# Performance work log

Measured on AMD Instinct MI355X. Metric: run time of the kernel, lower is better.

## Reference

```python
import jax, jax.numpy as jnp
import numpy as np

N = 16384
IN_FEATS = 128
HIDDEN = 128
OUT_FEATS = 64


def setup_inputs() -> dict:
    key = jax.random.key(0)
    ks = jax.random.split(key, 8)
    x = jax.random.normal(ks[0], (N, IN_FEATS), dtype=jnp.float32)
    adj = jax.random.uniform(ks[1], (N, N), dtype=jnp.float32)
    def glorot(k, shape):
        lim = 1.0 / np.sqrt(shape[0])
        return jax.random.uniform(k, shape, minval=-lim, maxval=lim, dtype=jnp.float32)
    W1 = glorot(ks[2], (IN_FEATS, HIDDEN))
    b1 = jnp.zeros((HIDDEN,), dtype=jnp.float32)
    W2 = glorot(ks[3], (HIDDEN, OUT_FEATS))
    b2 = jnp.zeros((OUT_FEATS,), dtype=jnp.float32)
    W_out = glorot(ks[4], (OUT_FEATS, 1))
    b_out = jnp.zeros((1,), dtype=jnp.float32)
    return {"x": x, "adj": adj, "W1": W1, "b1": b1, "W2": W2, "b2": b2,
            "W_out": W_out, "b_out": b_out}


def _gcn_layer(x, adj, W, b):
    # support = x @ W ; out = adj @ support + b  (standard GraphConvLayer)
    return adj @ (x @ W) + b


def reference(x, adj, W1, b1, W2, b2, W_out, b_out):
    h = jax.nn.relu(_gcn_layer(x, adj, W1, b1))      # [N, hidden]
    h = _gcn_layer(h, adj, W2, b2)                   # [N, out_feats]
    pooled = h.sum(axis=0)                           # [out_feats] graph readout
    return pooled @ W_out + b_out                    # [1]
```

## Files before the change

### kernel.cpp

```cpp
#include <hip/hip_runtime.h>
#include <hip/hip_bf16.h>
#include <stdint.h>

#define NN   16384
#define FI   128
#define FH   128
#define FO   64

#define BM   32
#define BK   64
#define LDK  72
#define KHALF (NN / 2)
#define NTH  (KHALF / BK)
#define NPART 512

typedef float f32x4 __attribute__((ext_vector_type(4)));
typedef short s16x8 __attribute__((ext_vector_type(8)));
typedef short s16x4 __attribute__((ext_vector_type(4)));

__device__ __forceinline__ unsigned short f2bf(float f) {
    union { float f; unsigned u; } v; v.f = f;
    unsigned u = v.u;
    return (unsigned short)((u + 0x7FFFu + ((u >> 16) & 1u)) >> 16);
}

__global__ __launch_bounds__(256) void k1_s1t(const float* __restrict__ x,
                                              const float* __restrict__ W1,
                                              unsigned short* __restrict__ S1T) {
    __shared__ float w1s[FI][FH];
    __shared__ float xs[64][132];

    const int t  = threadIdx.x;
    const int b  = blockIdx.x;
    const int k0 = b * 64;

    float* wflat = &w1s[0][0];
    for (int i = t; i < FI * FH; i += 256) wflat[i] = W1[i];

    #pragma unroll
    for (int s = 0; s < 8; ++s) {
        int idx = t + 256 * s;
        int r   = idx >> 5;
        int f4  = idx & 31;
        f32x4 vv = *(const f32x4*)(x + (size_t)(k0 + r) * FI + f4 * 4);
        *(f32x4*)(&xs[r][f4 * 4]) = vv;
    }
    __syncthreads();

    const int w = t >> 6;
    const int l = t & 63;

    float acc[32];
    #pragma unroll
    for (int j = 0; j < 32; ++j) acc[j] = 0.f;

    for (int f4 = 0; f4 < 32; ++f4) {
        f32x4 xv = *(const f32x4*)(&xs[l][f4 * 4]);
        #pragma unroll
        for (int e = 0; e < 4; ++e) {
            const int f = f4 * 4 + e;
            #pragma unroll
            for (int cth = 0; cth < 8; ++cth) {
                f32x4 wv = *(const f32x4*)(&w1s[f][w * 32 + cth * 4]);
                acc[cth * 4 + 0] += xv[e] * wv[0];
                acc[cth * 4 + 1] += xv[e] * wv[1];
                acc[cth * 4 + 2] += xv[e] * wv[2];
                acc[cth * 4 + 3] += xv[e] * wv[3];
            }
        }
    }

    const int k = k0 + l;
    #pragma unroll
    for (int j = 0; j < 32; ++j) {
        const int n = w * 32 + j;
        S1T[(size_t)n * NN + k] = f2bf(acc[j]);
    }
}

__global__ __launch_bounds__(256, 4) void k2_agg(const float* __restrict__ adj,
                                                 const unsigned short* __restrict__ S1T,
                                                 float* __restrict__ Tpart,
                                                 float* __restrict__ cpart) {
    __shared__ unsigned short aA[2][BM][LDK];
    __shared__ unsigned short bBs[FH][LDK];
    __shared__ float cs[4][BK];

    const int  t    = threadIdx.x;
    const int  rb   = blockIdx.x >> 1;
    const int  kh   = blockIdx.x & 1;
    const long m0   = (long)rb * BM;
    const long k0   = (long)kh * KHALF;
    const int  w    = t >> 6;
    const int  l    = t & 63;
    const int  ar   = t >> 4;
    const int  ac4  = t & 15;
    const int  sn   = t >> 3;
    const int  sch  = t & 7;
    const int  m    = l & 15;
    const int  quad = l >> 4;

    f32x4 acc[2][2];
    #pragma unroll
    for (int i = 0; i < 2; ++i)
        #pragma unroll
        for (int j = 0; j < 2; ++j) acc[i][j] = (f32x4){0.f, 0.f, 0.f, 0.f};

    f32x4 paX0, paX1, paY0, paY1;
    s16x8 psX[4], psY[4];

#define BAR() do {                                                                \
    asm volatile("s_waitcnt lgkmcnt(0)" ::: "memory");                            \
    __builtin_amdgcn_s_barrier();                                                 \
} while (0)

#define LOAD(PA0, PA1, PS, J) do {                                                \
    const long koff_ = k0 + (long)(J) * BK;                                       \
    PA0 = *(const f32x4*)(adj + (m0 + ar) * NN + koff_ + ac4 * 4);                \
    PA1 = *(const f32x4*)(adj + (m0 + ar + 16) * NN + koff_ + ac4 * 4);           \
    _Pragma("unroll")                                                             \
    for (int s_ = 0; s_ < 4; ++s_)                                                \
        PS[s_] = *(const s16x8*)(S1T + (size_t)(sn + 32 * s_) * NN + koff_ + sch * 8); \
} while (0)

#define CSUM_STAGEA(SB, PA0, PA1) do {                                            \
    f32x4 pv_;                                                                    \
    _Pragma("unroll")                                                             \
    for (int j_ = 0; j_ < 4; ++j_) {                                              \
        float p_ = PA0[j_] + PA1[j_];                                             \
        p_ += __shfl_xor(p_, 16);                                                 \
        p_ += __shfl_xor(p_, 32);                                                 \
        pv_[j_] = p_;                                                             \
    }                                                                             \
    if (l < 16) *(f32x4*)(&cs[w][l * 4]) = pv_;                                   \
    s16x4 q0_, q1_;                                                               \
    _Pragma("unroll")                                                             \
    for (int j_ = 0; j_ < 4; ++j_) {                                              \
        q0_[j_] = (short)f2bf(PA0[j_]);                                           \
        q1_[j_] = (short)f2bf(PA1[j_]);                                           \
    }                                                                             \
    *(s16x4*)(&aA[SB][ar][ac4 * 4])      = q0_;                                   \
    *(s16x4*)(&aA[SB][ar + 16][ac4 * 4]) = q1_;                                   \
} while (0)

#define STAGEB(PS) do {                                                           \
    _Pragma("unroll")                                                             \
    for (int s_ = 0; s_ < 4; ++s_)                                                \
        *(s16x8*)(&bBs[sn + 32 * s_][sch * 8]) = PS[s_];                          \
} while (0)

#define FLUSH(J) do {                                                             \
    if (t < BK)                                                                   \
        cpart[(size_t)rb * NN + k0 + (long)(J) * BK + t] =                        \
            cs[0][t] + cs[1][t] + cs[2][t] + cs[3][t];                            \
} while (0)

#define COMPUTE(SB) do {                                                          \
    _Pragma("unroll")                                                             \
    for (int ks = 0; ks < 2; ++ks) {                                              \
        s16x8 af_[2], bf_[2];                                                     \
        _Pragma("unroll")                                                         \
        for (int mt = 0; mt < 2; ++mt)                                            \
            af_[mt] = *(const s16x8*)(&aA[SB][mt * 16 + m][ks * 32 + quad * 8]);  \
        _Pragma("unroll")                                                         \
        for (int nt = 0; nt < 2; ++nt)                                            \
            bf_[nt] = *(const s16x8*)(&bBs[w * 32 + nt * 16 + m][ks * 32 + quad * 8]); \
        _Pragma("unroll")                                                         \
        for (int mt = 0; mt < 2; ++mt)                                            \
            _Pragma("unroll")                                                     \
            for (int nt = 0; nt < 2; ++nt)                                        \
                acc[mt][nt] = __builtin_amdgcn_mfma_f32_16x16x32_bf16(            \
                    af_[mt], bf_[nt], acc[mt][nt], 0, 0, 0);                      \
    }                                                                             \
} while (0)

    LOAD(paX0, paX1, psX, 0);
    LOAD(paY0, paY1, psY, 1);
    CSUM_STAGEA(0, paX0, paX1);
    STAGEB(psX);
    BAR();
    FLUSH(0);
    BAR();

    for (int j = 0; j < NTH; j += 2) {
        if (j + 2 < NTH) LOAD(paX0, paX1, psX, j + 2);
        COMPUTE(0);
        CSUM_STAGEA(1, paY0, paY1);
        BAR();
        STAGEB(psY);
        FLUSH(j + 1);
        BAR();

        if (j + 3 < NTH) LOAD(paY0, paY1, psY, j + 3);
        COMPUTE(1);
        if (j + 2 < NTH) CSUM_STAGEA(0, paX0, paX1);
        BAR();
        if (j + 2 < NTH) {
            STAGEB(psX);
            FLUSH(j + 2);
        }
        BAR();
    }

#undef BAR
#undef LOAD
#undef CSUM_STAGEA
#undef STAGEB
#undef FLUSH
#undef COMPUTE

    float* Tp = Tpart + (size_t)kh * NN * FH;
    #pragma unroll
    for (int mt = 0; mt < 2; ++mt)
        #pragma unroll
        for (int nt = 0; nt < 2; ++nt) {
            const int col = w * 32 + nt * 16 + m;
            #pragma unroll
            for (int r = 0; r < 4; ++r) {
                const long row = m0 + mt * 16 + quad * 4 + r;
                Tp[row * FH + col] = acc[mt][nt][r];
            }
        }
}

__global__ __launch_bounds__(256) void k3_v(const float* __restrict__ Tpart,
                                            const float* __restrict__ cpart,
                                            const float* __restrict__ b1,
                                            float* __restrict__ v) {
    __shared__ float vp[FH];
    __shared__ float cw[4][64];
    __shared__ float cloc[64];

    const int t = threadIdx.x;
    const int b = blockIdx.x;
    const int w = t >> 6;
    const int l = t & 63;

    float s = 0.f;
    #pragma unroll 8
    for (int i = 0; i < NPART / 4; ++i)
        s += cpart[(size_t)(w + 4 * i) * NN + b * 64 + l];
    cw[w][l] = s;
    if (t < FH) vp[t] = 0.f;
    __syncthreads();
    if (t < 64) cloc[t] = cw[0][t] + cw[1][t] + cw[2][t] + cw[3][t];
    __syncthreads();

    const int kk = t >> 2;
    const int mq = t & 3;
    const int k  = b * 64 + kk;
    const float ck = cloc[kk];

    #pragma unroll
    for (int j4 = 0; j4 < 8; ++j4) {
        f32x4 t0 = *(const f32x4*)(Tpart + (size_t)k * FH + mq * 32 + j4 * 4);
        f32x4 t1 = *(const f32x4*)(Tpart + ((size_t)NN + k) * FH + mq * 32 + j4 * 4);
        f32x4 bv = *(const f32x4*)(b1 + mq * 32 + j4 * 4);
        #pragma unroll
        for (int e = 0; e < 4; ++e) {
            float h = t0[e] + t1[e] + bv[e];
            h = h > 0.f ? h : 0.f;
            atomicAdd(&vp[mq * 32 + j4 * 4 + e], ck * h);
        }
    }
    __syncthreads();
    if (t < FH) atomicAdd(&v[t], vp[t]);
}

__global__ void k4_out(const float* __restrict__ v, const float* __restrict__ W2,
                       const float* __restrict__ b2, const float* __restrict__ Wout,
                       const float* __restrict__ bout, float* __restrict__ out) {
    const int j = threadIdx.x;
    float pj = (float)NN * b2[j];
    for (int mm = 0; mm < FH; ++mm) pj += v[mm] * W2[mm * FO + j];
    float s = pj * Wout[j];
    #pragma unroll
    for (int off = 32; off; off >>= 1) s += __shfl_down(s, off);
    if (j == 0) out[0] = s + bout[0];
}

extern "C" void kernel_launch(void* const* d_in, const int* in_sizes, int n_in,
                              void* d_out, int out_size, void* d_ws, size_t ws_size,
                              hipStream_t stream) {
    const float* x    = (const float*)d_in[0];
    const float* adj  = (const float*)d_in[1];
    const float* W1   = (const float*)d_in[2];
    const float* b1   = (const float*)d_in[3];
    const float* W2   = (const float*)d_in[4];
    const float* b2   = (const float*)d_in[5];
    const float* Wout = (const float*)d_in[6];
    const float* bout = (const float*)d_in[7];
    float* out = (float*)d_out;

    char* ws = (char*)d_ws;
    unsigned short* S1T = (unsigned short*)ws;
    float* Tpart = (float*)(ws + (4u  << 20));
    float* cpart = (float*)(ws + (20u << 20));
    float* v     = (float*)(ws + (52u << 20));

    hipMemsetAsync(v, 0, 512, stream);

    k1_s1t<<<256, 256, 0, stream>>>(x, W1, S1T);
    k2_agg<<<1024, 256, 0, stream>>>(adj, S1T, Tpart, cpart);
    k3_v  <<<256, 256, 0, stream>>>(Tpart, cpart, b1, v);
    k4_out<<<1, 64, 0, stream>>>(v, W2, b2, Wout, bout, out);
}
```

Measured before the change: 1.487 ms.

## Deepen k2 prefetch pipeline and double-buffer B tile, write per-wave column sums

Reworks the aggregation kernel's main loop into a four-stage register prefetch with double-buffered LDS for both the adjacency and S1T tiles. This allows one barrier per iteration instead of two. The LDS cross-wave column-sum reduction is removed. Each wave now writes its partial column sums straight to global memory, so cpart grows to 4x and NPART becomes 2048, and the workspace offset for v moves accordingly. The cost is more registers, with launch bounds occupancy lowered from 4 to 3, more LDS, and four times the cpart write and read traffic.

Result: slower. 1.569 ms (+5.5%).

```diff
diff --git a/kernel.cpp b/kernel.cpp
--- a/kernel.cpp
+++ b/kernel.cpp
@@ -12,7 +12,7 @@
 #define LDK  72
 #define KHALF (NN / 2)
 #define NTH  (KHALF / BK)
-#define NPART 512
+#define NPART 2048
 
 typedef float f32x4 __attribute__((ext_vector_type(4)));
 typedef short s16x8 __attribute__((ext_vector_type(8)));
@@ -78,13 +78,12 @@
     }
 }
 
-__global__ __launch_bounds__(256, 4) void k2_agg(const float* __restrict__ adj,
+__global__ __launch_bounds__(256, 3) void k2_agg(const float* __restrict__ adj,
                                                  const unsigned short* __restrict__ S1T,
                                                  float* __restrict__ Tpart,
                                                  float* __restrict__ cpart) {
     __shared__ unsigned short aA[2][BM][LDK];
-    __shared__ unsigned short bBs[FH][LDK];
-    __shared__ float cs[4][BK];
+    __shared__ unsigned short bB[2][FH][LDK];
 
     const int  t    = threadIdx.x;
     const int  rb   = blockIdx.x >> 1;
@@ -106,8 +105,8 @@
         #pragma unroll
         for (int j = 0; j < 2; ++j) acc[i][j] = (f32x4){0.f, 0.f, 0.f, 0.f};
 
-    f32x4 paX0, paX1, paY0, paY1;
-    s16x8 psX[4], psY[4];
+    f32x4 paW0, paW1, paX0, paX1, paY0, paY1, paZ0, paZ1;
+    s16x8 psW[4], psX[4], psY[4], psZ[4];
 
 #define BAR() do {                                                                \
     asm volatile("s_waitcnt lgkmcnt(0)" ::: "memory");                            \
@@ -123,7 +122,7 @@
         PS[s_] = *(const s16x8*)(S1T + (size_t)(sn + 32 * s_) * NN + koff_ + sch * 8); \
 } while (0)
 
-#define CSUM_STAGEA(SB, PA0, PA1) do {                                            \
+#define STAGE(SB, PA0, PA1, PS, J) do {                                           \
     f32x4 pv_;                                                                    \
     _Pragma("unroll")                                                             \
     for (int j_ = 0; j_ < 4; ++j_) {                                              \
@@ -132,7 +131,8 @@
         p_ += __shfl_xor(p_, 32);                                                 \
         pv_[j_] = p_;                                                             \
     }                                                                             \
-    if (l < 16) *(f32x4*)(&cs[w][l * 4]) = pv_;                                   \
+    if (l < 16)                                                                   \
+        *(f32x4*)(&cpart[((size_t)rb * 4 + w) * NN + k0 + (long)(J) * BK + l * 4]) = pv_; \
     s16x4 q0_, q1_;                                                               \
     _Pragma("unroll")                                                             \
     for (int j_ = 0; j_ < 4; ++j_) {                                              \
@@ -141,18 +141,9 @@
     }                                                                             \
     *(s16x4*)(&aA[SB][ar][ac4 * 4])      = q0_;                                   \
     *(s16x4*)(&aA[SB][ar + 16][ac4 * 4]) = q1_;                                   \
-} while (0)
-
-#define STAGEB(PS) do {                                                           \
     _Pragma("unroll")                                                             \
     for (int s_ = 0; s_ < 4; ++s_)                                                \
-        *(s16x8*)(&bBs[sn + 32 * s_][sch * 8]) = PS[s_];                          \
-} while (0)
-
-#define FLUSH(J) do {                                                             \
-    if (t < BK)                                                                   \
-        cpart[(size_t)rb * NN + k0 + (long)(J) * BK + t] =                        \
-            cs[0][t] + cs[1][t] + cs[2][t] + cs[3][t];                            \
+        *(s16x8*)(&bB[SB][sn + 32 * s_][sch * 8]) = PS[s_];                       \
 } while (0)
 
 #define COMPUTE(SB) do {                                                          \
@@ -164,7 +155,7 @@
             af_[mt] = *(const s16x8*)(&aA[SB][mt * 16 + m][ks * 32 + quad * 8]);  \
         _Pragma("unroll")                                                         \
         for (int nt = 0; nt < 2; ++nt)                                            \
-            bf_[nt] = *(const s16x8*)(&bBs[w * 32 + nt * 16 + m][ks * 32 + quad * 8]); \
+            bf_[nt] = *(const s16x8*)(&bB[SB][w * 32 + nt * 16 + m][ks * 32 + quad * 8]); \
         _Pragma("unroll")                                                         \
         for (int mt = 0; mt < 2; ++mt)                                            \
             _Pragma("unroll")                                                     \
@@ -174,40 +165,33 @@
     }                                                                             \
 } while (0)
 
-    LOAD(paX0, paX1, psX, 0);
-    LOAD(paY0, paY1, psY, 1);
-    CSUM_STAGEA(0, paX0, paX1);
-    STAGEB(psX);
+#define ITER(J, PA0, PA1, PS) do {                                                \
+    COMPUTE((J) & 1);                                                             \
+    if ((J) + 1 < NTH) STAGE(((J) + 1) & 1, PA0, PA1, PS, (J) + 1);               \
+    if ((J) + 5 < NTH) LOAD(PA0, PA1, PS, (J) + 5);                               \
+    BAR();                                                                        \
+} while (0)
+
+    LOAD(paW0, paW1, psW, 0);
+    LOAD(paX0, paX1, psX, 1);
+    LOAD(paY0, paY1, psY, 2);
+    LOAD(paZ0, paZ1, psZ, 3);
+    STAGE(0, paW0, paW1, psW, 0);
+    LOAD(paW0, paW1, psW, 4);
     BAR();
-    FLUSH(0);
-    BAR();
-
-    for (int j = 0; j < NTH; j += 2) {
-        if (j + 2 < NTH) LOAD(paX0, paX1, psX, j + 2);
-        COMPUTE(0);
-        CSUM_STAGEA(1, paY0, paY1);
-        BAR();
-        STAGEB(psY);
-        FLUSH(j + 1);
-        BAR();
-
-        if (j + 3 < NTH) LOAD(paY0, paY1, psY, j + 3);
-        COMPUTE(1);
-        if (j + 2 < NTH) CSUM_STAGEA(0, paX0, paX1);
-        BAR();
-        if (j + 2 < NTH) {
-            STAGEB(psX);
-            FLUSH(j + 2);
-        }
-        BAR();
+
+    for (int j = 0; j < NTH; j += 4) {
+        ITER(j + 0, paX0, paX1, psX);
+        ITER(j + 1, paY0, paY1, psY);
+        ITER(j + 2, paZ0, paZ1, psZ);
+        ITER(j + 3, paW0, paW1, psW);
     }
 
 #undef BAR
 #undef LOAD
-#undef CSUM_STAGEA
-#undef STAGEB
-#undef FLUSH
+#undef STAGE
 #undef COMPUTE
+#undef ITER
 
     float* Tp = Tpart + (size_t)kh * NN * FH;
     #pragma unroll
@@ -294,9 +278,9 @@
 
     char* ws = (char*)d_ws;
     unsigned short* S1T = (unsigned short*)ws;
-    float* Tpart = (float*)(ws + (4u  << 20));
-    float* cpart = (float*)(ws + (20u << 20));
-    float* v     = (float*)(ws + (52u << 20));
+    float* Tpart = (float*)(ws + (4u   << 20));
+    float* cpart = (float*)(ws + (20u  << 20));
+    float* v     = (float*)(ws + (148u << 20));
 
     hipMemsetAsync(v, 0, 512, stream);
 
```

## Double-buffer per-wave B tiles and column sums to halve barriers in aggregation loop

Applied to the files above, without the earlier changes.

The aggregation kernel now gives each wave its own double-buffered slice of the S1T tile and double-buffers the column-sum scratch. This lets staging of the next tile and the flush of the previous column sums overlap with MFMA compute, cutting the loop from four barriers per two tiles to two. Loads also run one tile further ahead. The larger shared memory footprint forces launch bounds down from 4 to 3 blocks per SM, which lowers occupancy.

After: 1.565 ms. 1.05x slower.

```diff
diff --git a/kernel.cpp b/kernel.cpp
--- a/kernel.cpp
+++ b/kernel.cpp
@@ -78,13 +78,13 @@
     }
 }
 
-__global__ __launch_bounds__(256, 4) void k2_agg(const float* __restrict__ adj,
+__global__ __launch_bounds__(256, 3) void k2_agg(const float* __restrict__ adj,
                                                  const unsigned short* __restrict__ S1T,
                                                  float* __restrict__ Tpart,
                                                  float* __restrict__ cpart) {
     __shared__ unsigned short aA[2][BM][LDK];
-    __shared__ unsigned short bBs[FH][LDK];
-    __shared__ float cs[4][BK];
+    __shared__ unsigned short bW[4][2][BM][LDK];
+    __shared__ float cs[2][4][BK];
 
     const int  t    = threadIdx.x;
     const int  rb   = blockIdx.x >> 1;
@@ -95,8 +95,8 @@
     const int  l    = t & 63;
     const int  ar   = t >> 4;
     const int  ac4  = t & 15;
-    const int  sn   = t >> 3;
-    const int  sch  = t & 7;
+    const int  br   = l >> 3;
+    const int  bc   = l & 7;
     const int  m    = l & 15;
     const int  quad = l >> 4;
 
@@ -119,11 +119,12 @@
     PA0 = *(const f32x4*)(adj + (m0 + ar) * NN + koff_ + ac4 * 4);                \
     PA1 = *(const f32x4*)(adj + (m0 + ar + 16) * NN + koff_ + ac4 * 4);           \
     _Pragma("unroll")                                                             \
-    for (int s_ = 0; s_ < 4; ++s_)                                                \
-        PS[s_] = *(const s16x8*)(S1T + (size_t)(sn + 32 * s_) * NN + koff_ + sch * 8); \
-} while (0)
-
-#define CSUM_STAGEA(SB, PA0, PA1) do {                                            \
+    for (int g_ = 0; g_ < 4; ++g_)                                                \
+        PS[g_] = *(const s16x8*)(S1T + (size_t)(w * 32 + g_ * 8 + br) * NN        \
+                                 + koff_ + bc * 8);                               \
+} while (0)
+
+#define STAGE(SB, PA0, PA1, PS) do {                                              \
     f32x4 pv_;                                                                    \
     _Pragma("unroll")                                                             \
     for (int j_ = 0; j_ < 4; ++j_) {                                              \
@@ -132,7 +133,7 @@
         p_ += __shfl_xor(p_, 32);                                                 \
         pv_[j_] = p_;                                                             \
     }                                                                             \
-    if (l < 16) *(f32x4*)(&cs[w][l * 4]) = pv_;                                   \
+    if (l < 16) *(f32x4*)(&cs[SB][w][l * 4]) = pv_;                               \
     s16x4 q0_, q1_;                                                               \
     _Pragma("unroll")                                                             \
     for (int j_ = 0; j_ < 4; ++j_) {                                              \
@@ -141,18 +142,15 @@
     }                                                                             \
     *(s16x4*)(&aA[SB][ar][ac4 * 4])      = q0_;                                   \
     *(s16x4*)(&aA[SB][ar + 16][ac4 * 4]) = q1_;                                   \
-} while (0)
-
-#define STAGEB(PS) do {                                                           \
-    _Pragma("unroll")                                                             \
-    for (int s_ = 0; s_ < 4; ++s_)                                                \
-        *(s16x8*)(&bBs[sn + 32 * s_][sch * 8]) = PS[s_];                          \
-} while (0)
-
-#define FLUSH(J) do {                                                             \
+    _Pragma("unroll")                                                             \
+    for (int g_ = 0; g_ < 4; ++g_)                                                \
+        *(s16x8*)(&bW[w][SB][g_ * 8 + br][bc * 8]) = PS[g_];                      \
+} while (0)
+
+#define FLUSH(SB, J) do {                                                         \
     if (t < BK)                                                                   \
         cpart[(size_t)rb * NN + k0 + (long)(J) * BK + t] =                        \
-            cs[0][t] + cs[1][t] + cs[2][t] + cs[3][t];                            \
+            cs[SB][0][t] + cs[SB][1][t] + cs[SB][2][t] + cs[SB][3][t];            \
 } while (0)
 
 #define COMPUTE(SB) do {                                                          \
@@ -164,7 +162,7 @@
             af_[mt] = *(const s16x8*)(&aA[SB][mt * 16 + m][ks * 32 + quad * 8]);  \
         _Pragma("unroll")                                                         \
         for (int nt = 0; nt < 2; ++nt)                                            \
-            bf_[nt] = *(const s16x8*)(&bBs[w * 32 + nt * 16 + m][ks * 32 + quad * 8]); \
+            bf_[nt] = *(const s16x8*)(&bW[w][SB][nt * 16 + m][ks * 32 + quad * 8]); \
         _Pragma("unroll")                                                         \
         for (int mt = 0; mt < 2; ++mt)                                            \
             _Pragma("unroll")                                                     \
@@ -176,36 +174,27 @@
 
     LOAD(paX0, paX1, psX, 0);
     LOAD(paY0, paY1, psY, 1);
-    CSUM_STAGEA(0, paX0, paX1);
-    STAGEB(psX);
+    STAGE(0, paX0, paX1, psX);
+    LOAD(paX0, paX1, psX, 2);
     BAR();
-    FLUSH(0);
-    BAR();
 
     for (int j = 0; j < NTH; j += 2) {
-        if (j + 2 < NTH) LOAD(paX0, paX1, psX, j + 2);
+        if (j + 1 < NTH) STAGE(1, paY0, paY1, psY);
+        FLUSH(0, j);
         COMPUTE(0);
-        CSUM_STAGEA(1, paY0, paY1);
+        if (j + 3 < NTH) LOAD(paY0, paY1, psY, j + 3);
         BAR();
-        STAGEB(psY);
-        FLUSH(j + 1);
-        BAR();
-
-        if (j + 3 < NTH) LOAD(paY0, paY1, psY, j + 3);
+
+        if (j + 2 < NTH) STAGE(0, paX0, paX1, psX);
+        FLUSH(1, j + 1);
         COMPUTE(1);
-        if (j + 2 < NTH) CSUM_STAGEA(0, paX0, paX1);
-        BAR();
-        if (j + 2 < NTH) {
-            STAGEB(psX);
-            FLUSH(j + 2);
-        }
+        if (j + 4 < NTH) LOAD(paX0, paX1, psX, j + 4);
         BAR();
     }
 
 #undef BAR
 #undef LOAD
-#undef CSUM_STAGEA
-#undef STAGEB
+#undef STAGE
 #undef FLUSH
 #undef COMPUTE
 
```
